# Kernel optimization log

Hardware: AMD Instinct MI355X
Metric: run time of the kernel (lower is better)

## Reference

```python
import jax, jax.numpy as jnp
import numpy as np

B, NPG, H, D = 8, 6250, 4, 128   # graphs, nodes/graph, heads, hidden
N = B * NPG                       # 50000 nodes total
E = 400000                        # edges
VOCAB = 10000


def setup_inputs() -> dict:
    key = jax.random.key(0)
    ks = jax.random.split(key, 12)
    p = lambda k, shape: jax.random.normal(k, shape, dtype=jnp.float32) * 0.05
    return {
        "node_ids": jax.random.randint(ks[0], (N,), 0, VOCAB),
        "src": jax.random.randint(ks[1], (E,), 0, N),
        "dst": jax.random.randint(ks[2], (E,), 0, N),
        "emb": p(ks[3], (VOCAB, D)),
        "W_src": p(ks[4], (D, H * D)), "b_src": jnp.zeros((H * D,), jnp.float32),
        "W_dst": p(ks[5], (D, H * D)), "b_dst": jnp.zeros((H * D,), jnp.float32),
        "attn": p(ks[6], (H, D)),
        "W_res": p(ks[7], (D, H * D)), "b_res": jnp.zeros((H * D,), jnp.float32),
        "W_gc": p(ks[8], (D, D)), "b_gc": jnp.zeros((D,), jnp.float32),
        "W_mlp": p(ks[9], (3 * D, 1)), "b_mlp": jnp.zeros((1,), jnp.float32),
    }


def _leaky(x, s):
    return jnp.where(x >= 0, x, s * x)


def _maxpool(feat):
    # dgl.max_nodes: per-graph max over nodes -> [B, feat_dim]
    return jnp.max(feat.reshape(B, NPG, -1), axis=1)


def _gatv2(x, src, dst, W_src, b_src, W_dst, b_dst, attn, W_res, b_res):
    # DGL GATv2Conv (share_weights=False, residual=True, eval mode -> no dropout)
    hs = (x @ W_src + b_src).reshape(N, H, D)
    hd = (x @ W_dst + b_dst).reshape(N, H, D)
    e = _leaky(hs[src] + hd[dst], 0.2)              # [E,H,D]
    logits = jnp.einsum('ehd,hd->eh', e, attn)      # [E,H]
    m = jax.ops.segment_max(logits, dst, num_segments=N)
    ex = jnp.exp(logits - m[dst])
    denom = jax.ops.segment_sum(ex, dst, num_segments=N)
    alpha = ex / denom[dst]                          # edge softmax per dst/head
    rst = jax.ops.segment_sum(hs[src] * alpha[..., None], dst, num_segments=N)
    rst = rst + (x @ W_res + b_res).reshape(N, H, D)
    return _leaky(rst, 0.01)                         # nn.LeakyReLU() activation


def _graphconv(x, src, dst, W, b):
    # DGL GraphConv norm='both', allow_zero_in_degree=True, LeakyReLU activation
    ones = jnp.ones((E,), x.dtype)
    dout = jnp.clip(jax.ops.segment_sum(ones, src, num_segments=N), 1.0, None)
    din = jnp.clip(jax.ops.segment_sum(ones, dst, num_segments=N), 1.0, None)
    h = x * jax.lax.rsqrt(dout)[:, None]
    agg = jax.ops.segment_sum(h[src], dst, num_segments=N)
    h = agg * jax.lax.rsqrt(din)[:, None]
    return _leaky(h @ W + b, 0.01)


def reference(node_ids, src, dst, emb, W_src, b_src, W_dst, b_dst, attn,
              W_res, b_res, W_gc, b_gc, W_mlp, b_mlp):
    feat = emb[node_ids]                             # featurize_nodes
    pools = [_maxpool(feat)]
    res = _gatv2(feat, src, dst, W_src, b_src, W_dst, b_dst, attn,
                 W_res, b_res).mean(axis=1)          # mean over heads -> [N,D]
    pools.append(_maxpool(res))
    res = _graphconv(res, src, dst, W_gc, b_gc)
    pools.append(_maxpool(res))
    agg = jnp.concatenate(pools, axis=1)             # [B, 3D]
    # reward_predictor_block_two: ReLU -> (Dropout eval) -> Linear(3D, 1)
    return jax.nn.relu(agg) @ W_mlp + b_mlp          # BCE logits [B,1]
```

## Files before the change

kernel.cpp:

```cpp
#include <hip/hip_runtime.h>
#include <float.h>
#include <math.h>

#define Bg   8
#define NPGc 6250
#define Hh   4
#define Dd   128
#define Nn   50000
#define Ee   400000
#define HDd  512
#define WNf  1536
#define NCHUNK 49

typedef unsigned short ushort_t;
typedef __attribute__((ext_vector_type(8))) short bf16x8;
typedef __attribute__((ext_vector_type(4))) float f32x4;
typedef __attribute__((ext_vector_type(2))) float f32x2;

__device__ __forceinline__ void atomicMaxF(float* addr, float val) {
    if (val >= 0.0f) atomicMax((int*)addr, __float_as_int(val));
    else             atomicMin((unsigned int*)addr, __float_as_uint(val));
}

__device__ __forceinline__ ushort_t f2bf(float x) {
    unsigned u = __float_as_uint(x);
    unsigned r = (u + 0x7FFFu + ((u >> 16) & 1u)) >> 16;
    return (ushort_t)r;
}

__device__ __forceinline__ f32x2 bfpair(unsigned u) {
    f32x2 r;
    r.x = __uint_as_float(u << 16);
    r.y = __uint_as_float(u & 0xFFFF0000u);
    return r;
}

__global__ void setup_kernel(const int* __restrict__ ids, const float* __restrict__ emb,
                             float* __restrict__ feat, ushort_t* __restrict__ feat_bf,
                             const float* __restrict__ W_src, const float* __restrict__ W_dst,
                             const float* __restrict__ W_res, const float* __restrict__ W_gc,
                             const float* __restrict__ b_src, const float* __restrict__ b_dst,
                             const float* __restrict__ b_res,
                             ushort_t* __restrict__ Wt, ushort_t* __restrict__ Wt_gc,
                             float* __restrict__ bias_f,
                             int* __restrict__ din_i, float* __restrict__ dout,
                             int* __restrict__ cursor, float* __restrict__ pools) {
    int i = blockIdx.x * blockDim.x + threadIdx.x;
    {
        int n = i >> 5, c = i & 31;
        int id = ids[n];
        float4 v = ((const float4*)emb)[(size_t)id * 32 + c];
        ((float4*)feat)[(size_t)n * 32 + c] = v;
        ushort4 b;
        b.x = f2bf(v.x); b.y = f2bf(v.y); b.z = f2bf(v.z); b.w = f2bf(v.w);
        ((ushort4*)feat_bf)[(size_t)n * 32 + c] = b;
    }
    if (i < Nn) { din_i[i] = 0; dout[i] = 0.0f; cursor[i] = 0; }
    if (i < Bg * 3 * Dd) pools[i] = -FLT_MAX;
    if (i < WNf * 128) {
        int c = i >> 7, k = i & 127;
        float v = (c < 512) ? W_src[k * 512 + c]
                : (c < 1024) ? W_dst[k * 512 + (c - 512)]
                             : W_res[k * 512 + (c - 1024)];
        Wt[i] = f2bf(v);
    } else if (i < WNf * 128 + 128 * 128) {
        int j = i - WNf * 128;
        int c = j >> 7, k = j & 127;
        Wt_gc[j] = f2bf(W_gc[k * 128 + c]);
    }
    if (i < WNf)
        bias_f[i] = (i < 512) ? b_src[i] : (i < 1024) ? b_dst[i - 512] : b_res[i - 1024];
}

__global__ void maxpool_kernel(const float* __restrict__ x, float* __restrict__ pools, int col_off) {
    int b = blockIdx.x, chunk = blockIdx.y, d = threadIdx.x;
    int i0 = chunk * 125, i1 = i0 + 125;
    float mx = -FLT_MAX;
    for (int i = i0; i < i1; ++i)
        mx = fmaxf(mx, x[((size_t)(b * NPGc + i)) * Dd + d]);
    atomicMaxF(&pools[b * (3 * Dd) + col_off + d], mx);
}

__global__ void maxpool_bf_kernel(const ushort_t* __restrict__ x, float* __restrict__ pools, int col_off) {
    int b = blockIdx.x, chunk = blockIdx.y, lane = threadIdx.x;
    int i0 = chunk * 125;
    f32x2 mx = {-FLT_MAX, -FLT_MAX};
    for (int i = 0; i < 125; ++i) {
        unsigned u = *(const unsigned*)(x + ((size_t)(b * NPGc + i0 + i)) * Dd + lane * 2);
        mx = __builtin_elementwise_max(mx, bfpair(u));
    }
    atomicMaxF(&pools[b * (3 * Dd) + col_off + lane * 2],     mx.x);
    atomicMaxF(&pools[b * (3 * Dd) + col_off + lane * 2 + 1], mx.y);
}

#define GNT 3
__global__ __launch_bounds__(256) void mfma_gemm_kernel(
    const ushort_t* __restrict__ A, const ushort_t* __restrict__ Wt,
    const float* __restrict__ bias, ushort_t* __restrict__ Ob,
    int n_rows, int WN)
{
    __shared__ ushort_t Cs[2][64 * 64];
    int bid = blockIdx.x;
    int lin = (bid & 7) * (gridDim.x >> 3) + (bid >> 3);
    int row0 = (lin >> 3) * 64;
    int ct0  = (lin & 7) * GNT;
    int w = threadIdx.x >> 6, lane = threadIdx.x & 63;
    int lrow = lane & 15, kg = lane >> 4;

    bf16x8 av[4][4];
    {
        const ushort_t* ap = A + (size_t)(row0 + lrow) * 128 + kg * 8;
        #pragma unroll
        for (int fi = 0; fi < 4; ++fi)
            #pragma unroll
            for (int ks = 0; ks < 4; ++ks)
                av[fi][ks] = *(const bf16x8*)(ap + fi * 16 * 128 + ks * 32);
    }
    bf16x8 wv[GNT][4];
    float4 bv[GNT];
    {
        const ushort_t* wp = Wt + (size_t)(ct0 * 64 + w * 16 + lrow) * 128 + kg * 8;
        #pragma unroll
        for (int ct = 0; ct < GNT; ++ct) {
            #pragma unroll
            for (int ks = 0; ks < 4; ++ks)
                wv[ct][ks] = *(const bf16x8*)(wp + (size_t)ct * 8192 + ks * 32);
            bv[ct] = *(const float4*)(bias + (ct0 + ct) * 64 + w * 16 + kg * 4);
        }
    }

    #pragma unroll
    for (int ct = 0; ct < GNT; ++ct) {
        f32x4 acc[4] = {};
        #pragma unroll
        for (int ks = 0; ks < 4; ++ks)
            #pragma unroll
            for (int fi = 0; fi < 4; ++fi)
                acc[fi] = __builtin_amdgcn_mfma_f32_16x16x32_bf16(wv[ct][ks], av[fi][ks], acc[fi], 0, 0, 0);

        ushort_t* cb = Cs[ct & 1];
        int cbase = w * 32 + kg * 8;
        #pragma unroll
        for (int fi = 0; fi < 4; ++fi) {
            float o0 = acc[fi][0] + bv[ct].x;
            float o1 = acc[fi][1] + bv[ct].y;
            float o2 = acc[fi][2] + bv[ct].z;
            float o3 = acc[fi][3] + bv[ct].w;
            unsigned q0, q1;
            asm("v_cvt_pk_bf16_f32 %0, %1, %2" : "=v"(q0) : "v"(o0), "v"(o1));
            asm("v_cvt_pk_bf16_f32 %0, %1, %2" : "=v"(q1) : "v"(o2), "v"(o3));
            int r = fi * 16 + lrow;
            int cbyte = cbase ^ ((r & 7) << 4);
            uint2 q; q.x = q0; q.y = q1;
            *(uint2*)((char*)cb + r * 128 + cbyte) = q;
        }
        __syncthreads();
        {
            int t = threadIdx.x;
            const char* cbr = (const char*)cb;
            #pragma unroll
            for (int h = 0; h < 2; ++h) {
                int r  = (h * 256 + t) >> 3;
                int ch = t & 7;
                int cbyte = (ch * 16) ^ ((r & 7) << 4);
                uint4 v = *(const uint4*)(cbr + r * 128 + cbyte);
                int grow = row0 + r;
                if (grow < n_rows)
                    *(uint4*)((char*)Ob + ((size_t)grow * WN + (ct0 + ct) * 64) * 2 + ch * 16) = v;
            }
        }
    }
}

__global__ __launch_bounds__(256) void mfma_gc_pool_kernel(
    const ushort_t* __restrict__ A, const ushort_t* __restrict__ Wt,
    const float* __restrict__ bias, float* __restrict__ pools)
{
    int g = blockIdx.x / 98, lb = blockIdx.x % 98;
    int row0 = g * NPGc + lb * 64;
    int w = threadIdx.x >> 6, lane = threadIdx.x & 63;
    int lrow = lane & 15, kg = lane >> 4;

    bf16x8 av[4][4];
    {
        const ushort_t* ap = A + (size_t)(row0 + lrow) * 128 + kg * 8;
        #pragma unroll
        for (int fi = 0; fi < 4; ++fi)
            #pragma unroll
            for (int ks = 0; ks < 4; ++ks)
                av[fi][ks] = *(const bf16x8*)(ap + fi * 16 * 128 + ks * 32);
    }

    #pragma unroll
    for (int ct = 0; ct < 2; ++ct) {
        bf16x8 wv[4];
        const ushort_t* wp = Wt + (size_t)(ct * 64 + w * 16 + lrow) * 128 + kg * 8;
        #pragma unroll
        for (int ks = 0; ks < 4; ++ks) wv[ks] = *(const bf16x8*)(wp + ks * 32);

        f32x4 acc[4] = {};
        #pragma unroll
        for (int ks = 0; ks < 4; ++ks)
            #pragma unroll
            for (int fi = 0; fi < 4; ++fi)
                acc[fi] = __builtin_amdgcn_mfma_f32_16x16x32_bf16(wv[ks], av[fi][ks], acc[fi], 0, 0, 0);

        int colb = ct * 64 + w * 16 + kg * 4;
        float4 bv4 = *(const float4*)(bias + colb);
        float mcol[4] = {-FLT_MAX, -FLT_MAX, -FLT_MAX, -FLT_MAX};
        #pragma unroll
        for (int fi = 0; fi < 4; ++fi) {
            int lr = lb * 64 + fi * 16 + lrow;
            bool valid = lr < NPGc;
            #pragma unroll
            for (int j = 0; j < 4; ++j) {
                float v = acc[fi][j] + ((const float*)&bv4)[j];
                v = v >= 0.0f ? v : 0.01f * v;
                if (valid) mcol[j] = fmaxf(mcol[j], v);
            }
        }
        #pragma unroll
        for (int j = 0; j < 4; ++j) {
            mcol[j] = fmaxf(mcol[j], __shfl_xor(mcol[j], 1));
            mcol[j] = fmaxf(mcol[j], __shfl_xor(mcol[j], 2));
            mcol[j] = fmaxf(mcol[j], __shfl_xor(mcol[j], 4));
            mcol[j] = fmaxf(mcol[j], __shfl_xor(mcol[j], 8));
        }
        if (lrow == 0) {
            #pragma unroll
            for (int j = 0; j < 4; ++j)
                atomicMaxF(&pools[g * (3 * Dd) + 2 * Dd + colb + j], mcol[j]);
        }
    }
}

__global__ void degree2_kernel(const int* __restrict__ src, const int* __restrict__ dst,
                               int* __restrict__ din_i, float* __restrict__ dout) {
    int e = blockIdx.x * blockDim.x + threadIdx.x;
    if (e >= Ee) return;
    atomicAdd(&din_i[dst[e]], 1);
    atomicAdd(&dout[src[e]], 1.0f);
}

__global__ __launch_bounds__(256) void scan_reduce_kernel(const int* __restrict__ din_i,
                                                          int* __restrict__ partials) {
    int b = blockIdx.x, t = threadIdx.x;
    int base = b * 1024 + t * 4;
    int s = 0;
    #pragma unroll
    for (int j = 0; j < 4; ++j) { int i = base + j; if (i < Nn) s += din_i[i]; }
    #pragma unroll
    for (int off = 32; off > 0; off >>= 1) s += __shfl_xor(s, off);
    __shared__ int wsum[4];
    if ((t & 63) == 0) wsum[t >> 6] = s;
    __syncthreads();
    if (t == 0) partials[b] = wsum[0] + wsum[1] + wsum[2] + wsum[3];
}

__global__ void scan_mid_kernel(int* __restrict__ partials, int* __restrict__ row_start) {
    if (threadIdx.x == 0) {
        int acc = 0;
        for (int i = 0; i < NCHUNK; ++i) { int v = partials[i]; partials[i] = acc; acc += v; }
        row_start[Nn] = acc;
    }
}

__global__ __launch_bounds__(256) void scan_final_kernel(const int* __restrict__ din_i,
                                                         const int* __restrict__ partials,
                                                         int* __restrict__ row_start,
                                                         float* __restrict__ din_f) {
    int b = blockIdx.x, t = threadIdx.x;
    int base = b * 1024 + t * 4;
    int v[4]; int s = 0;
    #pragma unroll
    for (int j = 0; j < 4; ++j) {
        v[j] = (base + j < Nn) ? din_i[base + j] : 0;
        s += v[j];
    }
    __shared__ int buf[256];
    buf[t] = s;
    __syncthreads();
    #pragma unroll
    for (int off = 1; off < 256; off <<= 1) {
        int x = (t >= off) ? buf[t - off] : 0;
        __syncthreads();
        buf[t] += x;
        __syncthreads();
    }
    int excl = buf[t] - s + partials[b];
    #pragma unroll
    for (int j = 0; j < 4; ++j) {
        if (base + j < Nn) {
            row_start[base + j] = excl;
            din_f[base + j] = (float)v[j];
            excl += v[j];
        }
    }
}

__global__ void scatter_kernel(const int* __restrict__ src, const int* __restrict__ dst,
                               const int* __restrict__ row_start, int* __restrict__ cursor,
                               int* __restrict__ csr_src) {
    int e = blockIdx.x * blockDim.x + threadIdx.x;
    if (e >= Ee) return;
    int d = dst[e];
    int slot = row_start[d] + atomicAdd(&cursor[d], 1);
    csr_src[slot] = src[e];
}

__global__ __launch_bounds__(256) void gat_fused_kernel(
    const ushort_t* __restrict__ h_all, const float* __restrict__ attn,
    const int* __restrict__ row_start, const int* __restrict__ csr_src,
    ushort_t* __restrict__ res_bf)
{
    int d = (blockIdx.x * 256 + threadIdx.x) >> 6;
    int lane = threadIdx.x & 63;
    if (d >= Nn) return;
    int e0 = row_start[d], e1 = row_start[d + 1];

    const f32x2 z2 = {0.0f, 0.0f};
    f32x2 hd0, hd1, hd2, hd3, at0, at1, at2, at3;
    {
        uint4 hr = *(const uint4*)(h_all + (size_t)d * WNf + 512 + lane * 8);
        hd0 = bfpair(hr.x); hd1 = bfpair(hr.y); hd2 = bfpair(hr.z); hd3 = bfpair(hr.w);
        float4 a0 = *(const float4*)(attn + lane * 8);
        float4 a1 = *(const float4*)(attn + lane * 8 + 4);
        at0.x = a0.x; at0.y = a0.y; at1.x = a0.z; at1.y = a0.w;
        at2.x = a1.x; at2.y = a1.y; at3.x = a1.z; at3.y = a1.w;
    }

    float denom = 0.0f;
    f32x2 ac0 = z2, ac1 = z2, ac2 = z2, ac3 = z2;

#define LOGIT_PRE(r, h0, h1, h2, h3, pout)                                            \
    {                                                                                 \
        h0 = bfpair(r.x); h1 = bfpair(r.y); h2 = bfpair(r.z); h3 = bfpair(r.w);       \
        f32x2 p2 = z2;                                                                \
        { f32x2 x = h0 + hd0;                                                         \
          p2 += (__builtin_elementwise_max(x, z2) + 0.2f * __builtin_elementwise_min(x, z2)) * at0; } \
        { f32x2 x = h1 + hd1;                                                         \
          p2 += (__builtin_elementwise_max(x, z2) + 0.2f * __builtin_elementwise_min(x, z2)) * at1; } \
        { f32x2 x = h2 + hd2;                                                         \
          p2 += (__builtin_elementwise_max(x, z2) + 0.2f * __builtin_elementwise_min(x, z2)) * at2; } \
        { f32x2 x = h3 + hd3;                                                         \
          p2 += (__builtin_elementwise_max(x, z2) + 0.2f * __builtin_elementwise_min(x, z2)) * at3; } \
        pout = p2.x + p2.y;                                                           \
    }

    int e = e0;
    for (; e + 4 <= e1; e += 4) {
        int sA = csr_src[e], sB = csr_src[e + 1], sC = csr_src[e + 2], sD = csr_src[e + 3];
        uint4 rA = *(const uint4*)(h_all + (size_t)sA * WNf + lane * 8);
        uint4 rB = *(const uint4*)(h_all + (size_t)sB * WNf + lane * 8);
        uint4 rC = *(const uint4*)(h_all + (size_t)sC * WNf + lane * 8);
        uint4 rD = *(const uint4*)(h_all + (size_t)sD * WNf + lane * 8);
        f32x2 hA0, hA1, hA2, hA3, hB0, hB1, hB2, hB3;
        f32x2 hC0, hC1, hC2, hC3, hD0, hD1, hD2, hD3;
        float pA, pB, pC, pD;
        LOGIT_PRE(rA, hA0, hA1, hA2, hA3, pA);
        LOGIT_PRE(rB, hB0, hB1, hB2, hB3, pB);
        LOGIT_PRE(rC, hC0, hC1, hC2, hC3, pC);
        LOGIT_PRE(rD, hD0, hD1, hD2, hD3, pD);
        pA += __shfl_xor(pA, 1); pB += __shfl_xor(pB, 1); pC += __shfl_xor(pC, 1); pD += __shfl_xor(pD, 1);
        pA += __shfl_xor(pA, 2); pB += __shfl_xor(pB, 2); pC += __shfl_xor(pC, 2); pD += __shfl_xor(pD, 2);
        pA += __shfl_xor(pA, 4); pB += __shfl_xor(pB, 4); pC += __shfl_xor(pC, 4); pD += __shfl_xor(pD, 4);
        pA += __shfl_xor(pA, 8); pB += __shfl_xor(pB, 8); pC += __shfl_xor(pC, 8); pD += __shfl_xor(pD, 8);
        float exA = __expf(fminf(fmaxf(pA, -40.0f), 40.0f));
        float exB = __expf(fminf(fmaxf(pB, -40.0f), 40.0f));
        float exC = __expf(fminf(fmaxf(pC, -40.0f), 40.0f));
        float exD = __expf(fminf(fmaxf(pD, -40.0f), 40.0f));
        denom += (exA + exB) + (exC + exD);
        ac0 += hA0 * exA + hB0 * exB + hC0 * exC + hD0 * exD;
        ac1 += hA1 * exA + hB1 * exB + hC1 * exC + hD1 * exD;
        ac2 += hA2 * exA + hB2 * exB + hC2 * exC + hD2 * exD;
        ac3 += hA3 * exA + hB3 * exB + hC3 * exC + hD3 * exD;
    }
    for (; e < e1; ++e) {
        int s = csr_src[e];
        uint4 r = *(const uint4*)(h_all + (size_t)s * WNf + lane * 8);
        f32x2 h0, h1, h2, h3;
        float p;
        LOGIT_PRE(r, h0, h1, h2, h3, p);
        p += __shfl_xor(p, 1); p += __shfl_xor(p, 2);
        p += __shfl_xor(p, 4); p += __shfl_xor(p, 8);
        float ex = __expf(fminf(fmaxf(p, -40.0f), 40.0f));
        denom += ex;
        ac0 += h0 * ex; ac1 += h1 * ex; ac2 += h2 * ex; ac3 += h3 * ex;
    }
#undef LOGIT_PRE

    float inv = (e1 > e0) ? 1.0f / denom : 0.0f;
    f32x2 rv0, rv1, rv2, rv3;
    {
        uint4 rr = *(const uint4*)(h_all + (size_t)d * WNf + 1024 + lane * 8);
        rv0 = bfpair(rr.x); rv1 = bfpair(rr.y); rv2 = bfpair(rr.z); rv3 = bfpair(rr.w);
    }
    float t[8];
    {
        f32x2 v0 = ac0 * inv + rv0, v1 = ac1 * inv + rv1;
        f32x2 v2 = ac2 * inv + rv2, v3 = ac3 * inv + rv3;
        f32x2 l0 = __builtin_elementwise_max(v0, z2) + 0.01f * __builtin_elementwise_min(v0, z2);
        f32x2 l1 = __builtin_elementwise_max(v1, z2) + 0.01f * __builtin_elementwise_min(v1, z2);
        f32x2 l2 = __builtin_elementwise_max(v2, z2) + 0.01f * __builtin_elementwise_min(v2, z2);
        f32x2 l3 = __builtin_elementwise_max(v3, z2) + 0.01f * __builtin_elementwise_min(v3, z2);
        t[0] = l0.x; t[1] = l0.y; t[2] = l1.x; t[3] = l1.y;
        t[4] = l2.x; t[5] = l2.y; t[6] = l3.x; t[7] = l3.y;
    }
    #pragma unroll
    for (int j = 0; j < 8; ++j) {
        t[j] += __shfl_xor(t[j], 16);
        t[j] += __shfl_xor(t[j], 32);
    }
    if (lane < 16) {
        float o0 = 0.25f * t[0], o1 = 0.25f * t[1], o2 = 0.25f * t[2], o3 = 0.25f * t[3];
        float o4 = 0.25f * t[4], o5 = 0.25f * t[5], o6 = 0.25f * t[6], o7 = 0.25f * t[7];
        unsigned q0, q1, q2, q3;
        asm("v_cvt_pk_bf16_f32 %0, %1, %2" : "=v"(q0) : "v"(o0), "v"(o1));
        asm("v_cvt_pk_bf16_f32 %0, %1, %2" : "=v"(q1) : "v"(o2), "v"(o3));
        asm("v_cvt_pk_bf16_f32 %0, %1, %2" : "=v"(q2) : "v"(o4), "v"(o5));
        asm("v_cvt_pk_bf16_f32 %0, %1, %2" : "=v"(q3) : "v"(o6), "v"(o7));
        uint4 qb; qb.x = q0; qb.y = q1; qb.z = q2; qb.w = q3;
        *(uint4*)(res_bf + (size_t)d * Dd + lane * 8) = qb;
    }
}

__global__ __launch_bounds__(256) void gc_gather_kernel(
    const ushort_t* __restrict__ res_bf, const int* __restrict__ row_start,
    const int* __restrict__ csr_src, const float* __restrict__ dout,
    const float* __restrict__ din, ushort_t* __restrict__ agg_bf)
{
    int d = (blockIdx.x * 256 + threadIdx.x) >> 6;
    int lane = threadIdx.x & 63;
    if (d >= Nn) return;
    int e0 = row_start[d], e1 = row_start[d + 1];
    const f32x2 z2 = {0.0f, 0.0f};
    f32x2 a2 = z2;
    int s0 = (e0 < e1) ? csr_src[e0] : 0;
    int s1 = (e0 + 1 < e1) ? csr_src[e0 + 1] : s0;
    float sc0 = 1.0f / sqrtf(fmaxf((e0 < e1) ? dout[s0] : 1.0f, 1.0f));
    float sc1 = 1.0f / sqrtf(fmaxf((e0 + 1 < e1) ? dout[s1] : 1.0f, 1.0f));
    unsigned u0 = *(const unsigned*)(res_bf + (size_t)s0 * Dd + lane * 2);
    unsigned u1 = *(const unsigned*)(res_bf + (size_t)s1 * Dd + lane * 2);
    for (int e = e0; e < e1; ++e) {
        int s2 = (e + 2 < e1) ? csr_src[e + 2] : s0;
        float sc2 = 1.0f / sqrtf(fmaxf(dout[s2], 1.0f));
        unsigned u2 = *(const unsigned*)(res_bf + (size_t)s2 * Dd + lane * 2);
        a2 += bfpair(u0) * sc0;
        u0 = u1; u1 = u2; sc0 = sc1; sc1 = sc2;
    }
    float scd = 1.0f / sqrtf(fmaxf(din[d], 1.0f));
    float ax = a2.x * scd, ay = a2.y * scd;
    unsigned q;
    asm("v_cvt_pk_bf16_f32 %0, %1, %2" : "=v"(q) : "v"(ax), "v"(ay));
    *(unsigned*)(agg_bf + (size_t)d * Dd + lane * 2) = q;
}

__global__ void final_kernel(const float* __restrict__ pools, const float* __restrict__ W_mlp,
                             const float* __restrict__ b_mlp, float* __restrict__ out) {
    int b = blockIdx.x, lane = threadIdx.x;
    float s = 0.0f;
    for (int j = lane; j < 3 * Dd; j += 64)
        s += fmaxf(pools[b * (3 * Dd) + j], 0.0f) * W_mlp[j];
    #pragma unroll
    for (int off = 32; off > 0; off >>= 1) s += __shfl_xor(s, off);
    if (lane == 0) out[b] = s + b_mlp[0];
}

extern "C" void kernel_launch(void* const* d_in, const int* in_sizes, int n_in,
                              void* d_out, int out_size, void* d_ws, size_t ws_size,
                              hipStream_t stream) {
    const int*   node_ids = (const int*)d_in[0];
    const int*   src      = (const int*)d_in[1];
    const int*   dst      = (const int*)d_in[2];
    const float* emb      = (const float*)d_in[3];
    const float* W_src    = (const float*)d_in[4];
    const float* b_src    = (const float*)d_in[5];
    const float* W_dst    = (const float*)d_in[6];
    const float* b_dst    = (const float*)d_in[7];
    const float* attn     = (const float*)d_in[8];
    const float* W_res    = (const float*)d_in[9];
    const float* b_res    = (const float*)d_in[10];
    const float* W_gc     = (const float*)d_in[11];
    const float* b_gc     = (const float*)d_in[12];
    const float* W_mlp    = (const float*)d_in[13];
    const float* b_mlp    = (const float*)d_in[14];
    float* out = (float*)d_out;

    char* w = (char*)d_ws;
    size_t off = 0;
    float*    feat    = (float*)(w + off);    off += (size_t)Nn * Dd * 4;
    ushort_t* feat_bf = (ushort_t*)(w + off); off += (size_t)(Nn + 64) * Dd * 2;
    ushort_t* h_all   = (ushort_t*)(w + off); off += (size_t)Nn * WNf * 2;
    ushort_t* Wt      = (ushort_t*)(w + off); off += (size_t)WNf * 128 * 2;
    ushort_t* Wt_gc   = (ushort_t*)(w + off); off += (size_t)128 * 128 * 2;
    float*    bias_f  = (float*)(w + off);    off += (size_t)WNf * 4;
    int*      csr_src = (int*)(w + off);      off += (size_t)Ee * 4;
    int*      row_st  = (int*)(w + off);      off += ((size_t)Nn + 4) * 4;
    int*      cursor  = (int*)(w + off);      off += (size_t)Nn * 4;
    int*      din_i   = (int*)(w + off);      off += (size_t)Nn * 4;
    float*    din_f   = (float*)(w + off);    off += (size_t)Nn * 4;
    float*    dout_f  = (float*)(w + off);    off += (size_t)Nn * 4;
    int*      partials= (int*)(w + off);      off += 64 * 4;
    float*    pools   = (float*)(w + off);    off += (size_t)Bg * 3 * Dd * 4;
    ushort_t* res_bf  = (ushort_t*)(w + off); off += (size_t)Nn * Dd * 2;

    ushort_t* agg_bf = h_all;

    setup_kernel<<<(Nn * 32) / 256, 256, 0, stream>>>(
        node_ids, emb, feat, feat_bf, W_src, W_dst, W_res, W_gc,
        b_src, b_dst, b_res, Wt, Wt_gc, bias_f, din_i, dout_f, cursor, pools);
    maxpool_kernel<<<dim3(Bg, 50), Dd, 0, stream>>>(feat, pools, 0);

    degree2_kernel<<<(Ee + 255) / 256, 256, 0, stream>>>(src, dst, din_i, dout_f);
    scan_reduce_kernel<<<NCHUNK, 256, 0, stream>>>(din_i, partials);
    scan_mid_kernel<<<1, 64, 0, stream>>>(partials, row_st);
    scan_final_kernel<<<NCHUNK, 256, 0, stream>>>(din_i, partials, row_st, din_f);
    scatter_kernel<<<(Ee + 255) / 256, 256, 0, stream>>>(src, dst, row_st, cursor, csr_src);

    mfma_gemm_kernel<<<((Nn + 63) / 64) * 8, 256, 0, stream>>>(
        feat_bf, Wt, bias_f, h_all, Nn, WNf);

    gat_fused_kernel<<<(Nn * 64) / 256, 256, 0, stream>>>(h_all, attn, row_st, csr_src, res_bf);
    maxpool_bf_kernel<<<dim3(Bg, 50), 64, 0, stream>>>(res_bf, pools, Dd);

    gc_gather_kernel<<<(Nn * 64) / 256, 256, 0, stream>>>(res_bf, row_st, csr_src, dout_f, din_f, agg_bf);
    mfma_gc_pool_kernel<<<Bg * 98, 256, 0, stream>>>(agg_bf, Wt_gc, b_gc, pools);

    final_kernel<<<Bg, 64, 0, stream>>>(pools, W_mlp, b_mlp, out);
}
```

Measured before the change: 374.1 us.

## Fuse dst/residual projection GEMM into GAT aggregation kernel via LDS

The large GEMM now computes only the source projection (512 columns). The dst and residual projections (1024 columns) are computed per 16-node block inside the GAT kernel with MFMA and staged in swizzled shared memory. This stops writing and rereading 1024 bf16 columns per node through global memory, and the gathered hs rows become denser (512-wide stride). In exchange each GAT block holds 32KB of LDS and runs a per-block GEMM before its edge loop, which may lower occupancy and serialise compute ahead of the gather.

New measurement: 410.3 us. 9.7% more time.

```diff
diff --git a/kernel.cpp b/kernel.cpp
--- a/kernel.cpp
+++ b/kernel.cpp
@@ -9,7 +9,6 @@
 #define Nn   50000
 #define Ee   400000
 #define HDd  512
-#define WNf  1536
 #define NCHUNK 49
 
 typedef unsigned short ushort_t;
@@ -41,8 +40,9 @@
                              const float* __restrict__ W_res, const float* __restrict__ W_gc,
                              const float* __restrict__ b_src, const float* __restrict__ b_dst,
                              const float* __restrict__ b_res,
-                             ushort_t* __restrict__ Wt, ushort_t* __restrict__ Wt_gc,
-                             float* __restrict__ bias_f,
+                             ushort_t* __restrict__ Wt_s, ushort_t* __restrict__ Wt_dr,
+                             ushort_t* __restrict__ Wt_gc,
+                             float* __restrict__ bias_s, float* __restrict__ bias_dr,
                              int* __restrict__ din_i, float* __restrict__ dout,
                              int* __restrict__ cursor, float* __restrict__ pools) {
     int i = blockIdx.x * blockDim.x + threadIdx.x;
@@ -57,19 +57,21 @@
     }
     if (i < Nn) { din_i[i] = 0; dout[i] = 0.0f; cursor[i] = 0; }
     if (i < Bg * 3 * Dd) pools[i] = -FLT_MAX;
-    if (i < WNf * 128) {
+    if (i < 512 * 128) {
         int c = i >> 7, k = i & 127;
-        float v = (c < 512) ? W_src[k * 512 + c]
-                : (c < 1024) ? W_dst[k * 512 + (c - 512)]
-                             : W_res[k * 512 + (c - 1024)];
-        Wt[i] = f2bf(v);
-    } else if (i < WNf * 128 + 128 * 128) {
-        int j = i - WNf * 128;
+        Wt_s[i] = f2bf(W_src[k * 512 + c]);
+    } else if (i < 512 * 128 + 1024 * 128) {
+        int j = i - 512 * 128;
+        int c = j >> 7, k = j & 127;
+        float v = (c < 512) ? W_dst[k * 512 + c] : W_res[k * 512 + (c - 512)];
+        Wt_dr[j] = f2bf(v);
+    } else if (i < 512 * 128 + 1024 * 128 + 128 * 128) {
+        int j = i - (512 * 128 + 1024 * 128);
         int c = j >> 7, k = j & 127;
         Wt_gc[j] = f2bf(W_gc[k * 128 + c]);
     }
-    if (i < WNf)
-        bias_f[i] = (i < 512) ? b_src[i] : (i < 1024) ? b_dst[i - 512] : b_res[i - 1024];
+    if (i < 512) bias_s[i] = b_src[i];
+    if (i < 1024) bias_dr[i] = (i < 512) ? b_dst[i] : b_res[i - 512];
 }
 
 __global__ void maxpool_kernel(const float* __restrict__ x, float* __restrict__ pools, int col_off) {
@@ -93,7 +95,7 @@
     atomicMaxF(&pools[b * (3 * Dd) + col_off + lane * 2 + 1], mx.y);
 }
 
-#define GNT 3
+template<int GNT, int NCS>
 __global__ __launch_bounds__(256) void mfma_gemm_kernel(
     const ushort_t* __restrict__ A, const ushort_t* __restrict__ Wt,
     const float* __restrict__ bias, ushort_t* __restrict__ Ob,
@@ -102,8 +104,8 @@
     __shared__ ushort_t Cs[2][64 * 64];
     int bid = blockIdx.x;
     int lin = (bid & 7) * (gridDim.x >> 3) + (bid >> 3);
-    int row0 = (lin >> 3) * 64;
-    int ct0  = (lin & 7) * GNT;
+    int row0 = (lin / NCS) * 64;
+    int ct0  = (lin % NCS) * GNT;
     int w = threadIdx.x >> 6, lane = threadIdx.x & 63;
     int lrow = lane & 15, kg = lane >> 4;
 
@@ -309,32 +311,73 @@
 }
 
 __global__ __launch_bounds__(256) void gat_fused_kernel(
-    const ushort_t* __restrict__ h_all, const float* __restrict__ attn,
+    const ushort_t* __restrict__ feat_bf, const ushort_t* __restrict__ hs,
+    const ushort_t* __restrict__ Wt_dr, const float* __restrict__ bias_dr,
+    const float* __restrict__ attn,
     const int* __restrict__ row_start, const int* __restrict__ csr_src,
     ushort_t* __restrict__ res_bf)
 {
-    int d = (blockIdx.x * 256 + threadIdx.x) >> 6;
-    int lane = threadIdx.x & 63;
-    if (d >= Nn) return;
-    int e0 = row_start[d], e1 = row_start[d + 1];
+    __shared__ char HD[16 * 2048];
+    int nb = blockIdx.x * 16;
+    int w = threadIdx.x >> 6, lane = threadIdx.x & 63;
+    int lrow = lane & 15, kg = lane >> 4;
+
+    {
+        bf16x8 av[4];
+        const ushort_t* ap = feat_bf + (size_t)(nb + lrow) * 128 + kg * 8;
+        #pragma unroll
+        for (int ks = 0; ks < 4; ++ks) av[ks] = *(const bf16x8*)(ap + ks * 32);
+        #pragma unroll 4
+        for (int cf = 0; cf < 16; ++cf) {
+            int col0 = w * 256 + cf * 16;
+            bf16x8 wv[4];
+            const ushort_t* wp = Wt_dr + (size_t)(col0 + lrow) * 128 + kg * 8;
+            #pragma unroll
+            for (int ks = 0; ks < 4; ++ks) wv[ks] = *(const bf16x8*)(wp + ks * 32);
+            f32x4 acc = {};
+            #pragma unroll
+            for (int ks = 0; ks < 4; ++ks)
+                acc = __builtin_amdgcn_mfma_f32_16x16x32_bf16(wv[ks], av[ks], acc, 0, 0, 0);
+            int colb = col0 + kg * 4;
+            float4 bv = *(const float4*)(bias_dr + colb);
+            float o0 = acc[0] + bv.x, o1 = acc[1] + bv.y;
+            float o2 = acc[2] + bv.z, o3 = acc[3] + bv.w;
+            unsigned q0, q1;
+            asm("v_cvt_pk_bf16_f32 %0, %1, %2" : "=v"(q0) : "v"(o0), "v"(o1));
+            asm("v_cvt_pk_bf16_f32 %0, %1, %2" : "=v"(q1) : "v"(o2), "v"(o3));
+            int byte = (colb * 2) ^ ((lrow & 7) << 4);
+            uint2 q; q.x = q0; q.y = q1;
+            *(uint2*)(HD + lrow * 2048 + byte) = q;
+        }
+    }
+    __syncthreads();
 
     const f32x2 z2 = {0.0f, 0.0f};
-    f32x2 hd0, hd1, hd2, hd3, at0, at1, at2, at3;
+    f32x2 at0, at1, at2, at3;
     {
-        uint4 hr = *(const uint4*)(h_all + (size_t)d * WNf + 512 + lane * 8);
-        hd0 = bfpair(hr.x); hd1 = bfpair(hr.y); hd2 = bfpair(hr.z); hd3 = bfpair(hr.w);
         float4 a0 = *(const float4*)(attn + lane * 8);
         float4 a1 = *(const float4*)(attn + lane * 8 + 4);
         at0.x = a0.x; at0.y = a0.y; at1.x = a0.z; at1.y = a0.w;
         at2.x = a1.x; at2.y = a1.y; at3.x = a1.z; at3.y = a1.w;
     }
 
-    float denom = 0.0f;
-    f32x2 ac0 = z2, ac1 = z2, ac2 = z2, ac3 = z2;
-
-#define LOGIT_PRE(r, h0, h1, h2, h3, pout)                                            \
+    for (int i = 0; i < 4; ++i) {
+        int r = w * 4 + i;
+        int d = nb + r;
+        int e0 = row_start[d], e1 = row_start[d + 1];
+
+        f32x2 hd0, hd1, hd2, hd3;
+        {
+            uint4 hr = *(const uint4*)(HD + r * 2048 + ((lane * 16) ^ ((r & 7) << 4)));
+            hd0 = bfpair(hr.x); hd1 = bfpair(hr.y); hd2 = bfpair(hr.z); hd3 = bfpair(hr.w);
+        }
+
+        float denom = 0.0f;
+        f32x2 ac0 = z2, ac1 = z2, ac2 = z2, ac3 = z2;
+
+#define LOGIT_PRE(rr, h0, h1, h2, h3, pout)                                           \
     {                                                                                 \
-        h0 = bfpair(r.x); h1 = bfpair(r.y); h2 = bfpair(r.z); h3 = bfpair(r.w);       \
+        h0 = bfpair(rr.x); h1 = bfpair(rr.y); h2 = bfpair(rr.z); h3 = bfpair(rr.w);   \
         f32x2 p2 = z2;                                                                \
         { f32x2 x = h0 + hd0;                                                         \
           p2 += (__builtin_elementwise_max(x, z2) + 0.2f * __builtin_elementwise_min(x, z2)) * at0; } \
@@ -347,80 +390,81 @@
         pout = p2.x + p2.y;                                                           \
     }
 
-    int e = e0;
-    for (; e + 4 <= e1; e += 4) {
-        int sA = csr_src[e], sB = csr_src[e + 1], sC = csr_src[e + 2], sD = csr_src[e + 3];
-        uint4 rA = *(const uint4*)(h_all + (size_t)sA * WNf + lane * 8);
-        uint4 rB = *(const uint4*)(h_all + (size_t)sB * WNf + lane * 8);
-        uint4 rC = *(const uint4*)(h_all + (size_t)sC * WNf + lane * 8);
-        uint4 rD = *(const uint4*)(h_all + (size_t)sD * WNf + lane * 8);
-        f32x2 hA0, hA1, hA2, hA3, hB0, hB1, hB2, hB3;
-        f32x2 hC0, hC1, hC2, hC3, hD0, hD1, hD2, hD3;
-        float pA, pB, pC, pD;
-        LOGIT_PRE(rA, hA0, hA1, hA2, hA3, pA);
-        LOGIT_PRE(rB, hB0, hB1, hB2, hB3, pB);
-        LOGIT_PRE(rC, hC0, hC1, hC2, hC3, pC);
-        LOGIT_PRE(rD, hD0, hD1, hD2, hD3, pD);
-        pA += __shfl_xor(pA, 1); pB += __shfl_xor(pB, 1); pC += __shfl_xor(pC, 1); pD += __shfl_xor(pD, 1);
-        pA += __shfl_xor(pA, 2); pB += __shfl_xor(pB, 2); pC += __shfl_xor(pC, 2); pD += __shfl_xor(pD, 2);
-        pA += __shfl_xor(pA, 4); pB += __shfl_xor(pB, 4); pC += __shfl_xor(pC, 4); pD += __shfl_xor(pD, 4);
-        pA += __shfl_xor(pA, 8); pB += __shfl_xor(pB, 8); pC += __shfl_xor(pC, 8); pD += __shfl_xor(pD, 8);
-        float exA = __expf(fminf(fmaxf(pA, -40.0f), 40.0f));
-        float exB = __expf(fminf(fmaxf(pB, -40.0f), 40.0f));
-        float exC = __expf(fminf(fmaxf(pC, -40.0f), 40.0f));
-        float exD = __expf(fminf(fmaxf(pD, -40.0f), 40.0f));
-        denom += (exA + exB) + (exC + exD);
-        ac0 += hA0 * exA + hB0 * exB + hC0 * exC + hD0 * exD;
-        ac1 += hA1 * exA + hB1 * exB + hC1 * exC + hD1 * exD;
-        ac2 += hA2 * exA + hB2 * exB + hC2 * exC + hD2 * exD;
-        ac3 += hA3 * exA + hB3 * exB + hC3 * exC + hD3 * exD;
-    }
-    for (; e < e1; ++e) {
-        int s = csr_src[e];
-        uint4 r = *(const uint4*)(h_all + (size_t)s * WNf + lane * 8);
-        f32x2 h0, h1, h2, h3;
-        float p;
-        LOGIT_PRE(r, h0, h1, h2, h3, p);
-        p += __shfl_xor(p, 1); p += __shfl_xor(p, 2);
-        p += __shfl_xor(p, 4); p += __shfl_xor(p, 8);
-        float ex = __expf(fminf(fmaxf(p, -40.0f), 40.0f));
-        denom += ex;
-        ac0 += h0 * ex; ac1 += h1 * ex; ac2 += h2 * ex; ac3 += h3 * ex;
-    }
+        int e = e0;
+        for (; e + 4 <= e1; e += 4) {
+            int sA = csr_src[e], sB = csr_src[e + 1], sC = csr_src[e + 2], sD = csr_src[e + 3];
+            uint4 rA = *(const uint4*)(hs + (size_t)sA * HDd + lane * 8);
+            uint4 rB = *(const uint4*)(hs + (size_t)sB * HDd + lane * 8);
+            uint4 rC = *(const uint4*)(hs + (size_t)sC * HDd + lane * 8);
+            uint4 rD = *(const uint4*)(hs + (size_t)sD * HDd + lane * 8);
+            f32x2 hA0, hA1, hA2, hA3, hB0, hB1, hB2, hB3;
+            f32x2 hC0, hC1, hC2, hC3, hD0, hD1, hD2, hD3;
+            float pA, pB, pC, pD;
+            LOGIT_PRE(rA, hA0, hA1, hA2, hA3, pA);
+            LOGIT_PRE(rB, hB0, hB1, hB2, hB3, pB);
+            LOGIT_PRE(rC, hC0, hC1, hC2, hC3, pC);
+            LOGIT_PRE(rD, hD0, hD1, hD2, hD3, pD);
+            pA += __shfl_xor(pA, 1); pB += __shfl_xor(pB, 1); pC += __shfl_xor(pC, 1); pD += __shfl_xor(pD, 1);
+            pA += __shfl_xor(pA, 2); pB += __shfl_xor(pB, 2); pC += __shfl_xor(pC, 2); pD += __shfl_xor(pD, 2);
+            pA += __shfl_xor(pA, 4); pB += __shfl_xor(pB, 4); pC += __shfl_xor(pC, 4); pD += __shfl_xor(pD, 4);
+            pA += __shfl_xor(pA, 8); pB += __shfl_xor(pB, 8); pC += __shfl_xor(pC, 8); pD += __shfl_xor(pD, 8);
+            float exA = __expf(fminf(fmaxf(pA, -40.0f), 40.0f));
+            float exB = __expf(fminf(fmaxf(pB, -40.0f), 40.0f));
+            float exC = __expf(fminf(fmaxf(pC, -40.0f), 40.0f));
+            float exD = __expf(fminf(fmaxf(pD, -40.0f), 40.0f));
+            denom += (exA + exB) + (exC + exD);
+            ac0 += hA0 * exA + hB0 * exB + hC0 * exC + hD0 * exD;
+            ac1 += hA1 * exA + hB1 * exB + hC1 * exC + hD1 * exD;
+            ac2 += hA2 * exA + hB2 * exB + hC2 * exC + hD2 * exD;
+            ac3 += hA3 * exA + hB3 * exB + hC3 * exC + hD3 * exD;
+        }
+        for (; e < e1; ++e) {
+            int s = csr_src[e];
+            uint4 rr = *(const uint4*)(hs + (size_t)s * HDd + lane * 8);
+            f32x2 h0, h1, h2, h3;
+            float p;
+            LOGIT_PRE(rr, h0, h1, h2, h3, p);
+            p += __shfl_xor(p, 1); p += __shfl_xor(p, 2);
+            p += __shfl_xor(p, 4); p += __shfl_xor(p, 8);
+            float ex = __expf(fminf(fmaxf(p, -40.0f), 40.0f));
+            denom += ex;
+            ac0 += h0 * ex; ac1 += h1 * ex; ac2 += h2 * ex; ac3 += h3 * ex;
+        }
 #undef LOGIT_PRE
 
-    float inv = (e1 > e0) ? 1.0f / denom : 0.0f;
-    f32x2 rv0, rv1, rv2, rv3;
-    {
-        uint4 rr = *(const uint4*)(h_all + (size_t)d * WNf + 1024 + lane * 8);
-        rv0 = bfpair(rr.x); rv1 = bfpair(rr.y); rv2 = bfpair(rr.z); rv3 = bfpair(rr.w);
-    }
-    float t[8];
-    {
-        f32x2 v0 = ac0 * inv + rv0, v1 = ac1 * inv + rv1;
-        f32x2 v2 = ac2 * inv + rv2, v3 = ac3 * inv + rv3;
-        f32x2 l0 = __builtin_elementwise_max(v0, z2) + 0.01f * __builtin_elementwise_min(v0, z2);
-        f32x2 l1 = __builtin_elementwise_max(v1, z2) + 0.01f * __builtin_elementwise_min(v1, z2);
-        f32x2 l2 = __builtin_elementwise_max(v2, z2) + 0.01f * __builtin_elementwise_min(v2, z2);
-        f32x2 l3 = __builtin_elementwise_max(v3, z2) + 0.01f * __builtin_elementwise_min(v3, z2);
-        t[0] = l0.x; t[1] = l0.y; t[2] = l1.x; t[3] = l1.y;
-        t[4] = l2.x; t[5] = l2.y; t[6] = l3.x; t[7] = l3.y;
-    }
-    #pragma unroll
-    for (int j = 0; j < 8; ++j) {
-        t[j] += __shfl_xor(t[j], 16);
-        t[j] += __shfl_xor(t[j], 32);
-    }
-    if (lane < 16) {
-        float o0 = 0.25f * t[0], o1 = 0.25f * t[1], o2 = 0.25f * t[2], o3 = 0.25f * t[3];
-        float o4 = 0.25f * t[4], o5 = 0.25f * t[5], o6 = 0.25f * t[6], o7 = 0.25f * t[7];
-        unsigned q0, q1, q2, q3;
-        asm("v_cvt_pk_bf16_f32 %0, %1, %2" : "=v"(q0) : "v"(o0), "v"(o1));
-        asm("v_cvt_pk_bf16_f32 %0, %1, %2" : "=v"(q1) : "v"(o2), "v"(o3));
-        asm("v_cvt_pk_bf16_f32 %0, %1, %2" : "=v"(q2) : "v"(o4), "v"(o5));
-        asm("v_cvt_pk_bf16_f32 %0, %1, %2" : "=v"(q3) : "v"(o6), "v"(o7));
-        uint4 qb; qb.x = q0; qb.y = q1; qb.z = q2; qb.w = q3;
-        *(uint4*)(res_bf + (size_t)d * Dd + lane * 8) = qb;
+        float inv = (e1 > e0) ? 1.0f / denom : 0.0f;
+        f32x2 rv0, rv1, rv2, rv3;
+        {
+            uint4 rr = *(const uint4*)(HD + r * 2048 + ((1024 + lane * 16) ^ ((r & 7) << 4)));
+            rv0 = bfpair(rr.x); rv1 = bfpair(rr.y); rv2 = bfpair(rr.z); rv3 = bfpair(rr.w);
+        }
+        float t[8];
+        {
+            f32x2 v0 = ac0 * inv + rv0, v1 = ac1 * inv + rv1;
+            f32x2 v2 = ac2 * inv + rv2, v3 = ac3 * inv + rv3;
+            f32x2 l0 = __builtin_elementwise_max(v0, z2) + 0.01f * __builtin_elementwise_min(v0, z2);
+            f32x2 l1 = __builtin_elementwise_max(v1, z2) + 0.01f * __builtin_elementwise_min(v1, z2);
+            f32x2 l2 = __builtin_elementwise_max(v2, z2) + 0.01f * __builtin_elementwise_min(v2, z2);
+            f32x2 l3 = __builtin_elementwise_max(v3, z2) + 0.01f * __builtin_elementwise_min(v3, z2);
+            t[0] = l0.x; t[1] = l0.y; t[2] = l1.x; t[3] = l1.y;
+            t[4] = l2.x; t[5] = l2.y; t[6] = l3.x; t[7] = l3.y;
+        }
+        #pragma unroll
+        for (int j = 0; j < 8; ++j) {
+            t[j] += __shfl_xor(t[j], 16);
+            t[j] += __shfl_xor(t[j], 32);
+        }
+        if (lane < 16) {
+            float o0 = 0.25f * t[0], o1 = 0.25f * t[1], o2 = 0.25f * t[2], o3 = 0.25f * t[3];
+            float o4 = 0.25f * t[4], o5 = 0.25f * t[5], o6 = 0.25f * t[6], o7 = 0.25f * t[7];
+            unsigned q0, q1, q2, q3;
+            asm("v_cvt_pk_bf16_f32 %0, %1, %2" : "=v"(q0) : "v"(o0), "v"(o1));
+            asm("v_cvt_pk_bf16_f32 %0, %1, %2" : "=v"(q1) : "v"(o2), "v"(o3));
+            asm("v_cvt_pk_bf16_f32 %0, %1, %2" : "=v"(q2) : "v"(o4), "v"(o5));
+            asm("v_cvt_pk_bf16_f32 %0, %1, %2" : "=v"(q3) : "v"(o6), "v"(o7));
+            uint4 qb; qb.x = q0; qb.y = q1; qb.z = q2; qb.w = q3;
+            *(uint4*)(res_bf + (size_t)d * Dd + lane * 8) = qb;
+        }
     }
 }
 
@@ -490,10 +534,12 @@
     size_t off = 0;
     float*    feat    = (float*)(w + off);    off += (size_t)Nn * Dd * 4;
     ushort_t* feat_bf = (ushort_t*)(w + off); off += (size_t)(Nn + 64) * Dd * 2;
-    ushort_t* h_all   = (ushort_t*)(w + off); off += (size_t)Nn * WNf * 2;
-    ushort_t* Wt      = (ushort_t*)(w + off); off += (size_t)WNf * 128 * 2;
+    ushort_t* hs_buf  = (ushort_t*)(w + off); off += (size_t)Nn * HDd * 2;
+    ushort_t* Wt_s    = (ushort_t*)(w + off); off += (size_t)512 * 128 * 2;
+    ushort_t* Wt_dr   = (ushort_t*)(w + off); off += (size_t)1024 * 128 * 2;
     ushort_t* Wt_gc   = (ushort_t*)(w + off); off += (size_t)128 * 128 * 2;
-    float*    bias_f  = (float*)(w + off);    off += (size_t)WNf * 4;
+    float*    bias_s  = (float*)(w + off);    off += 512 * 4;
+    float*    bias_dr = (float*)(w + off);    off += 1024 * 4;
     int*      csr_src = (int*)(w + off);      off += (size_t)Ee * 4;
     int*      row_st  = (int*)(w + off);      off += ((size_t)Nn + 4) * 4;
     int*      cursor  = (int*)(w + off);      off += (size_t)Nn * 4;
@@ -504,11 +550,12 @@
     float*    pools   = (float*)(w + off);    off += (size_t)Bg * 3 * Dd * 4;
     ushort_t* res_bf  = (ushort_t*)(w + off); off += (size_t)Nn * Dd * 2;
 
-    ushort_t* agg_bf = h_all;
+    ushort_t* agg_bf = hs_buf;
 
     setup_kernel<<<(Nn * 32) / 256, 256, 0, stream>>>(
         node_ids, emb, feat, feat_bf, W_src, W_dst, W_res, W_gc,
-        b_src, b_dst, b_res, Wt, Wt_gc, bias_f, din_i, dout_f, cursor, pools);
+        b_src, b_dst, b_res, Wt_s, Wt_dr, Wt_gc, bias_s, bias_dr,
+        din_i, dout_f, cursor, pools);
     maxpool_kernel<<<dim3(Bg, 50), Dd, 0, stream>>>(feat, pools, 0);
 
     degree2_kernel<<<(Ee + 255) / 256, 256, 0, stream>>>(src, dst, din_i, dout_f);
@@ -517,10 +564,11 @@
     scan_final_kernel<<<NCHUNK, 256, 0, stream>>>(din_i, partials, row_st, din_f);
     scatter_kernel<<<(Ee + 255) / 256, 256, 0, stream>>>(src, dst, row_st, cursor, csr_src);
 
-    mfma_gemm_kernel<<<((Nn + 63) / 64) * 8, 256, 0, stream>>>(
-        feat_bf, Wt, bias_f, h_all, Nn, WNf);
-
-    gat_fused_kernel<<<(Nn * 64) / 256, 256, 0, stream>>>(h_all, attn, row_st, csr_src, res_bf);
+    mfma_gemm_kernel<2, 4><<<((Nn + 63) / 64) * 4, 256, 0, stream>>>(
+        feat_bf, Wt_s, bias_s, hs_buf, Nn, HDd);
+
+    gat_fused_kernel<<<Nn / 16, 256, 0, stream>>>(
+        feat_bf, hs_buf, Wt_dr, bias_dr, attn, row_st, csr_src, res_bf);
     maxpool_bf_kernel<<<dim3(Bg, 50), 64, 0, stream>>>(res_bf, pools, Dd);
 
     gc_gather_kernel<<<(Nn * 64) / 256, 256, 0, stream>>>(res_bf, row_st, csr_src, dout_f, din_f, agg_bf);
```
